# Performance work log

Measured on AMD Instinct MI355X. Metric: run time of the kernel, lower is better.

Reference implementation:

```python
import jax, jax.numpy as jnp
import numpy as np

NUM_HEADS = 16
QKV_FEATURES = 2048
HEAD_DIM = QKV_FEATURES // NUM_HEADS
THETA = 10000.0


def compute_freqs_cis(dim, length, start_pos=0, theta=THETA, dtype=jnp.float32):
    freqs = 1.0 / theta ** (jnp.arange(0, dim, 2, dtype=jnp.float32) / dim)
    t = jnp.arange(length, dtype=jnp.float32) + start_pos
    freqs = jnp.outer(t, freqs)  # (L, dim//2)
    return jnp.sin(freqs).astype(dtype), jnp.cos(freqs).astype(dtype)


def apply_rotary_emb(x, sin, cos):
    # x: (B, L, H, D); sin/cos: (L, D//2); interleaved-pair rotation
    x1 = x[..., 0::2]
    x2 = x[..., 1::2]
    sin = sin[None, :, None, :]
    cos = cos[None, :, None, :]
    y1 = x1 * cos - x2 * sin
    y2 = x1 * sin + x2 * cos
    return jnp.stack([y1, y2], axis=-1).reshape(x.shape)


def setup_inputs() -> dict:
    key = jax.random.key(0)
    ks = jax.random.split(key, 6)
    B, L, E = 2, 2048, 2048
    s_in = 1.0 / np.sqrt(E)
    s_out = 1.0 / np.sqrt(QKV_FEATURES)
    return {
        "x": jax.random.normal(ks[0], (B, L, E), jnp.float32),
        "Wq": jax.random.normal(ks[1], (E, QKV_FEATURES), jnp.float32) * s_in,
        "Wk": jax.random.normal(ks[2], (E, QKV_FEATURES), jnp.float32) * s_in,
        "Wv": jax.random.normal(ks[3], (E, QKV_FEATURES), jnp.float32) * s_in,
        "Wo": jax.random.normal(ks[4], (QKV_FEATURES, E), jnp.float32) * s_out,
        "bo": jnp.zeros((E,), jnp.float32),
    }


def reference(x, Wq, Wk, Wv, Wo, bo):
    B, L, E = x.shape
    H, D = NUM_HEADS, HEAD_DIM

    q = (x @ Wq).reshape(B, L, H, D)
    k = (x @ Wk).reshape(B, L, H, D)
    v = (x @ Wv).reshape(B, L, H, D)

    sin, cos = compute_freqs_cis(D, L)
    q = apply_rotary_emb(q, sin, cos)
    k = apply_rotary_emb(k, sin, cos)

    scale = D ** (-0.5)
    sim = jnp.einsum("bqhd,bkhd->bhqk", q, k) * scale

    pos = jnp.arange(L)
    causal_mask = pos[None, :] <= pos[:, None]  # (Lq, Lk)
    sim = jnp.where(causal_mask[None, None, :, :], sim, -1e9)

    attn = jax.nn.softmax(sim, axis=-1)
    out = jnp.einsum("bhqk,bkhd->bqhd", attn, v).reshape(B, L, H * D)
    return out @ Wo + bo
```

## Files before the change

### kernel.cpp

```cpp
#include <hip/hip_runtime.h>
#include <hip/hip_bf16.h>
#include <stdint.h>
#include <stddef.h>

#define B_   2
#define L_   2048
#define E_   2048
#define H_   16
#define D_   128
#define F_   2048
#define NROW (B_*L_)
#define QS   6144

typedef __bf16 bf16_t;
typedef __bf16 bf16x4 __attribute__((ext_vector_type(4)));
typedef __bf16 bf16x8 __attribute__((ext_vector_type(8)));
typedef float  f32x4  __attribute__((ext_vector_type(4)));

__device__ __forceinline__ void gload16(const void* g, void* l) {
  __builtin_amdgcn_global_load_lds(
      (const __attribute__((address_space(1))) void*)g,
      (__attribute__((address_space(3))) void*)l, 16, 0, 0);
}

__global__ __launch_bounds__(256) void k_convert(const float* __restrict__ in,
                                                 bf16_t* __restrict__ out, int n4) {
  int i = blockIdx.x*256 + threadIdx.x;
  if (i >= n4) return;
  float4 v = ((const float4*)in)[i];
  bf16x4 t;
  t[0] = (__bf16)v.x; t[1] = (__bf16)v.y; t[2] = (__bf16)v.z; t[3] = (__bf16)v.w;
  ((bf16x4*)out)[i] = t;
}

__global__ __launch_bounds__(256) void k_transpose_w(const float* __restrict__ in,
                                                     bf16_t* __restrict__ out) {
  __shared__ float tile[32][33];
  const int ct = blockIdx.x, rt = blockIdx.y;
  const int c = threadIdx.x & 31, r0 = threadIdx.x >> 5;
  #pragma unroll
  for (int k = 0; k < 4; k++) {
    int r = r0 + k*8;
    tile[r][c] = in[(size_t)(rt*32 + r)*2048 + ct*32 + c];
  }
  __syncthreads();
  #pragma unroll
  for (int k = 0; k < 4; k++) {
    int r = r0 + k*8;
    out[(size_t)(ct*32 + r)*2048 + rt*32 + c] = (__bf16)tile[c][r];
  }
}

__global__ __launch_bounds__(256) void k_sincos(float2* __restrict__ sc) {
  int id = blockIdx.x*256 + threadIdx.x;
  int t = id >> 6, i = id & 63;
  float freq = powf(10000.0f, -(float)i / 64.0f);
  float a = (float)t * freq;
  sc[id] = make_float2(cosf(a), sinf(a));
}

__global__ __launch_bounds__(256) void k_rope(bf16_t* __restrict__ qk,
                                              const float2* __restrict__ sc,
                                              float scale, int n4) {
  int i = blockIdx.x*256 + threadIdx.x;
  if (i >= n4) return;
  int e  = i << 2;
  int d  = e & (F_-1);
  int ii = (d & (D_-1)) >> 1;
  int r  = e >> 11;
  int t  = r & (L_-1);
  bf16_t* p = qk + (size_t)r*QS + d;
  bf16x4 v = *(const bf16x4*)p;
  float2 cs0 = sc[t*64 + ii];
  float2 cs1 = sc[t*64 + ii + 1];
  cs0.x *= scale; cs0.y *= scale; cs1.x *= scale; cs1.y *= scale;
  float x0 = (float)v[0], x1 = (float)v[1], x2 = (float)v[2], x3 = (float)v[3];
  bf16x4 o;
  o[0] = (__bf16)(x0*cs0.x - x1*cs0.y);
  o[1] = (__bf16)(x0*cs0.y + x1*cs0.x);
  o[2] = (__bf16)(x2*cs1.x - x3*cs1.y);
  o[3] = (__bf16)(x2*cs1.y + x3*cs1.x);
  *(bf16x4*)p = o;
}

__global__ __launch_bounds__(256) void k_transpose_v(const bf16_t* __restrict__ in,
                                                     bf16_t* __restrict__ out) {
  __shared__ bf16_t tile[32][33];
  const int lt = blockIdx.x, dt = blockIdx.y, bh = blockIdx.z;
  const int b = bh >> 4;
  const int h = bh & 15;
  const int c = threadIdx.x & 31, r0 = threadIdx.x >> 5;
  #pragma unroll
  for (int k = 0; k < 4; k++) {
    int r = r0 + k*8;
    tile[r][c] = in[(size_t)(b*L_ + lt*32 + r)*QS + h*D_ + dt*32 + c];
  }
  __syncthreads();
  #pragma unroll
  for (int k = 0; k < 4; k++) {
    int r = r0 + k*8;
    out[(size_t)(bh*D_ + dt*32 + r)*L_ + lt*32 + c] = tile[c][r];
  }
}

template<typename OutT, bool BIAS>
__global__ __launch_bounds__(256) void k_gemm_bt(const bf16_t* __restrict__ A,
                                                 const bf16_t* __restrict__ BT,
                                                 OutT* __restrict__ C,
                                                 const float* __restrict__ bias,
                                                 int M, int N, int K) {
  __shared__ bf16_t As[128*64];
  __shared__ bf16_t Bs[128*64];
  const int tid  = threadIdx.x;
  const int lane = tid & 63, wave = tid >> 6;
  const int wr = wave >> 1, wc = wave & 1;
  const int nbx = N >> 7, nwg = nbx * (M >> 7);
  int bid = blockIdx.x;
  const int cpx = nwg >> 3;
  bid = (bid & 7)*cpx + (bid >> 3);
  const int bx = bid % nbx, by = bid / nbx;
  const int row0 = by*128, col0 = bx*128;
  const int sr  = tid >> 3;
  const int sxe = ((tid & 7) ^ (sr & 7)) << 3;
  const bf16_t* Ag = A  + (size_t)(row0 + sr)*K + sxe;
  const bf16_t* Bg = BT + (size_t)(col0 + sr)*K + sxe;
  char* AsB = (char*)As; char* BsB = (char*)Bs;
  const int lr = lane & 15, lg = lane >> 4;
  f32x4 acc[4][4] = {};
  for (int kt = 0; kt < K; kt += 64) {
    #pragma unroll
    for (int i = 0; i < 4; i++) {
      gload16(Ag + (size_t)i*32*K + kt, AsB + i*4096 + wave*1024);
      gload16(Bg + (size_t)i*32*K + kt, BsB + i*4096 + wave*1024);
    }
    __syncthreads();
    #pragma unroll
    for (int kd = 0; kd < 2; kd++) {
      bf16x8 af[4], bb[4];
      #pragma unroll
      for (int m = 0; m < 4; m++) {
        const int row = wr*64 + m*16 + lr;
        af[m] = *(const bf16x8*)(AsB + row*128 + (((kd*4 + lg) ^ (lr & 7)) << 4));
      }
      #pragma unroll
      for (int n = 0; n < 4; n++) {
        const int row = wc*64 + n*16 + lr;
        bb[n] = *(const bf16x8*)(BsB + row*128 + (((kd*4 + lg) ^ (lr & 7)) << 4));
      }
      __builtin_amdgcn_s_setprio(1);
      #pragma unroll
      for (int m = 0; m < 4; m++)
        #pragma unroll
        for (int n = 0; n < 4; n++)
          acc[m][n] = __builtin_amdgcn_mfma_f32_16x16x32_bf16(af[m], bb[n], acc[m][n], 0, 0, 0);
      __builtin_amdgcn_s_setprio(0);
    }
    __syncthreads();
  }
  #pragma unroll
  for (int m = 0; m < 4; m++) {
    #pragma unroll
    for (int n = 0; n < 4; n++) {
      const int col = col0 + wc*64 + n*16 + lr;
      const float bv = BIAS ? bias[col] : 0.0f;
      #pragma unroll
      for (int j = 0; j < 4; j++) {
        const int row = row0 + wr*64 + m*16 + lg*4 + j;
        C[(size_t)row*N + col] = (OutT)(acc[m][n][j] + bv);
      }
    }
  }
}

template<bool MASK>
__device__ __forceinline__ void attn_tile(
    int kv0, int wq0, int lr, int lg,
    const char* __restrict__ Kb, const char* __restrict__ Vb, char* __restrict__ Pb,
    const bf16x8 (&aq)[4], f32x4 (&o)[8], float& mrow, float& lsum) {
  const int swz = (lr & 7) << 4;
  f32x4 s[4] = {};
  #pragma unroll
  for (int kd = 0; kd < 4; kd++) {
    bf16x8 ak[4];
    #pragma unroll
    for (int n = 0; n < 4; n++)
      ak[n] = *(const bf16x8*)(Kb + (n*16 + lr)*256 + (((kd*4 + lg) << 4) ^ swz));
    __builtin_amdgcn_s_setprio(1);
    #pragma unroll
    for (int n = 0; n < 4; n++)
      s[n] = __builtin_amdgcn_mfma_f32_16x16x32_bf16(ak[n], aq[kd], s[n], 0, 0, 0);
    __builtin_amdgcn_s_setprio(0);
  }
  if (MASK) {
    const int q = wq0 + lr;
    #pragma unroll
    for (int n = 0; n < 4; n++)
      #pragma unroll
      for (int j = 0; j < 4; j++)
        if (kv0 + n*16 + lg*4 + j > q) s[n][j] = -30000.0f;
  }
  float pmax = fmaxf(
      fmaxf(fmaxf(fmaxf(s[0][0], s[0][1]), fmaxf(s[0][2], s[0][3])),
            fmaxf(fmaxf(s[1][0], s[1][1]), fmaxf(s[1][2], s[1][3]))),
      fmaxf(fmaxf(fmaxf(s[2][0], s[2][1]), fmaxf(s[2][2], s[2][3])),
            fmaxf(fmaxf(s[3][0], s[3][1]), fmaxf(s[3][2], s[3][3]))));
  pmax = fmaxf(pmax, __shfl_xor(pmax, 16));
  pmax = fmaxf(pmax, __shfl_xor(pmax, 32));
  if (!__all(pmax - mrow <= 8.0f)) {
    const float mnew = fmaxf(mrow, pmax);
    const float corr = exp2f(mrow - mnew);
    mrow = mnew;
    lsum *= corr;
    #pragma unroll
    for (int n2 = 0; n2 < 8; n2++) o[n2] *= corr;
  }
  float rs = 0.0f;
  #pragma unroll
  for (int n = 0; n < 4; n++)
    #pragma unroll
    for (int j = 0; j < 4; j++) {
      float p = exp2f(s[n][j] - mrow);
      s[n][j] = p;
      rs += p;
    }
  rs += __shfl_xor(rs, 16);
  rs += __shfl_xor(rs, 32);
  lsum += rs;
  #pragma unroll
  for (int n = 0; n < 4; n++) {
    bf16x4 pw;
    pw[0] = (__bf16)s[n][0]; pw[1] = (__bf16)s[n][1];
    pw[2] = (__bf16)s[n][2]; pw[3] = (__bf16)s[n][3];
    *(bf16x4*)(Pb + ((lr*128 + n*32 + lg*8) ^ swz)) = pw;
  }
  #pragma unroll
  for (int ks = 0; ks < 2; ks++) {
    bf16x8 pb = *(const bf16x8*)(Pb + ((lr*128 + ks*64 + lg*16) ^ swz));
    __builtin_amdgcn_s_setprio(1);
    #pragma unroll
    for (int n2 = 0; n2 < 8; n2++) {
      bf16x8 av = *(const bf16x8*)(Vb + (n2*16 + lr)*128 + (((ks*4 + lg) << 4) ^ swz));
      o[n2] = __builtin_amdgcn_mfma_f32_16x16x32_bf16(av, pb, o[n2], 0, 0, 0);
    }
    __builtin_amdgcn_s_setprio(0);
  }
}

__global__ __launch_bounds__(512, 4) void k_attn(const bf16_t* __restrict__ QKV,
                                                 const bf16_t* __restrict__ Vt,
                                                 bf16_t* __restrict__ O) {
  __shared__ bf16_t Ks[2][64*128];
  __shared__ bf16_t Vs[2][128*64];
  __shared__ bf16_t Pl[8][16*64];
  const int tid = threadIdx.x, lane = tid & 63, wave = tid >> 6;
  const int qt = (int)gridDim.x - 1 - (int)blockIdx.x;
  const int h = blockIdx.y, b = blockIdx.z;
  const int wq0 = qt*128 + wave*16;
  const int lr = lane & 15, lg = lane >> 4;
  char* Pb = (char*)&Pl[wave][0];
  const bf16_t* Q = QKV;
  const bf16_t* K = QKV + F_;

  bf16x8 aq[4];
  #pragma unroll
  for (int kd = 0; kd < 4; kd++)
    aq[kd] = *(const bf16x8*)&Q[(size_t)(b*L_ + wq0 + lr)*QS + h*D_ + kd*32 + lg*8];

  const int kr = tid >> 4, kc = tid & 15;
  const bf16_t* Kg0 = K + (size_t)(b*L_ + kr)*QS + h*D_ + ((kc ^ (kr & 7)) << 3);
  const int vr = tid >> 3, vc = tid & 7;
  const bf16_t* Vg0 = Vt + (size_t)((b*H_ + h)*D_ + vr)*L_ + ((vc ^ (vr & 7)) << 3);

  f32x4 o[8] = {};
  float mrow = -3.0e38f, lsum = 0.0f;
  const int ntb   = 2*qt + 2;
  const int nfull = (wq0 + 1) >> 6;
  const int nmine = ((wq0 + 15) >> 6) + 1;

  {
    char* kb = (char*)&Ks[0][0] + wave*1024;
    char* vb = (char*)&Vs[0][0] + wave*1024;
    gload16(Kg0,                    kb);
    gload16(Kg0 + (size_t)32*QS,    kb + 8192);
    gload16(Vg0,                    vb);
    gload16(Vg0 + (size_t)64*L_,    vb + 8192);
  }
  __syncthreads();

  int buf = 0;
  for (int t = 0; t < ntb; t++) {
    if (t + 1 < ntb) {
      const int kn = (t+1)*64;
      char* kb = (char*)&Ks[buf^1][0] + wave*1024;
      char* vb = (char*)&Vs[buf^1][0] + wave*1024;
      const bf16_t* kg = Kg0 + (size_t)kn*QS;
      const bf16_t* vg = Vg0 + kn;
      gload16(kg,                 kb);
      gload16(kg + (size_t)32*QS, kb + 8192);
      gload16(vg,                 vb);
      gload16(vg + (size_t)64*L_, vb + 8192);
    }
    const char* Kb = (const char*)&Ks[buf][0];
    const char* Vb = (const char*)&Vs[buf][0];
    if (t < nfull)
      attn_tile<false>(t*64, wq0, lr, lg, Kb, Vb, Pb, aq, o, mrow, lsum);
    else if (t < nmine)
      attn_tile<true >(t*64, wq0, lr, lg, Kb, Vb, Pb, aq, o, mrow, lsum);
    __syncthreads();
    buf ^= 1;
  }
  const float inv = 1.0f / lsum;
  bf16_t* orow = O + (size_t)(b*L_ + wq0 + lr)*F_ + h*D_ + lg*4;
  #pragma unroll
  for (int n2 = 0; n2 < 8; n2++) {
    bf16x4 ov;
    ov[0] = (__bf16)(o[n2][0]*inv); ov[1] = (__bf16)(o[n2][1]*inv);
    ov[2] = (__bf16)(o[n2][2]*inv); ov[3] = (__bf16)(o[n2][3]*inv);
    *(bf16x4*)(orow + n2*16) = ov;
  }
}

extern "C" void kernel_launch(void* const* d_in, const int* in_sizes, int n_in,
                              void* d_out, int out_size, void* d_ws, size_t ws_size,
                              hipStream_t stream) {
  const float* x  = (const float*)d_in[0];
  const float* Wq = (const float*)d_in[1];
  const float* Wk = (const float*)d_in[2];
  const float* Wv = (const float*)d_in[3];
  const float* Wo = (const float*)d_in[4];
  const float* bo = (const float*)d_in[5];
  float* out = (float*)d_out;

  char* ws = (char*)d_ws;
  size_t off = 0;
  auto alloc = [&](size_t bytes) {
    char* p = ws + off;
    off = (off + bytes + 255) & ~(size_t)255;
    return p;
  };
  bf16_t* xb    = (bf16_t*)alloc((size_t)NROW*E_*2);
  bf16_t* wqkvt = (bf16_t*)alloc((size_t)3*F_*E_*2);
  bf16_t* wot   = (bf16_t*)alloc((size_t)F_*E_*2);
  float2* sc    = (float2*)alloc((size_t)L_*64*sizeof(float2));
  bf16_t* qkv   = (bf16_t*)alloc((size_t)NROW*QS*2);
  bf16_t* vt    = (bf16_t*)alloc((size_t)NROW*F_*2);
  bf16_t* ob    = xb;

  const float scale2 = 0.08838834764831845f * 1.44269504088896f;

  k_convert<<<dim3((NROW*E_/4 + 255)/256), 256, 0, stream>>>(x, xb, NROW*E_/4);
  k_transpose_w<<<dim3(64, 64), 256, 0, stream>>>(Wq, wqkvt);
  k_transpose_w<<<dim3(64, 64), 256, 0, stream>>>(Wk, wqkvt + (size_t)F_*E_);
  k_transpose_w<<<dim3(64, 64), 256, 0, stream>>>(Wv, wqkvt + (size_t)2*F_*E_);
  k_transpose_w<<<dim3(64, 64), 256, 0, stream>>>(Wo, wot);
  k_sincos<<<dim3(L_*64/256), 256, 0, stream>>>(sc);

  k_gemm_bt<bf16_t, false><<<dim3((QS/128)*(NROW/128)), 256, 0, stream>>>(
      xb, wqkvt, qkv, nullptr, NROW, QS, E_);

  k_rope<<<dim3((NROW*F_/4 + 255)/256), 256, 0, stream>>>(qkv,      sc, scale2, NROW*F_/4);
  k_rope<<<dim3((NROW*F_/4 + 255)/256), 256, 0, stream>>>(qkv + F_, sc, 1.0f,   NROW*F_/4);
  k_transpose_v<<<dim3(L_/32, D_/32, B_*H_), 256, 0, stream>>>(qkv + 2*F_, vt);

  k_attn<<<dim3(L_/128, H_, B_), 512, 0, stream>>>(qkv, vt, ob);

  k_gemm_bt<float, true><<<dim3((E_/128)*(NROW/128)), 256, 0, stream>>>(
      ob, wot, out, bo, NROW, E_, F_);
}
```

Measured before the change: 438.8 us.

## Triple-buffer GEMM K-loop with async LDS loads and merge small launches

The bf16 GEMM is restructured to use a 32-wide K step with a three-stage LDS ring buffer, issuing global-to-LDS loads two steps ahead and waiting with explicit vmcnt counts instead of a full sync per tile. Occupancy is hinted at three blocks per CU, and the LDS swizzle is adjusted to the narrower rows. Separately, the four weight-transpose launches are merged into one 3D grid and the two RoPE launches into one kernel, cutting launch overhead. The hand-written waitcnt and barrier scheme relies on the exact number of outstanding loads, so a miscount would break correctness.

New measurement: 443.3 us. No clear change (+1.0%).

```diff
diff --git a/kernel.cpp b/kernel.cpp
--- a/kernel.cpp
+++ b/kernel.cpp
@@ -23,6 +23,8 @@
       (__attribute__((address_space(3))) void*)l, 16, 0, 0);
 }
 
+#define VMC(n)  asm volatile("s_waitcnt vmcnt(" #n ")" ::: "memory")
+
 __global__ __launch_bounds__(256) void k_convert(const float* __restrict__ in,
                                                  bf16_t* __restrict__ out, int n4) {
   int i = blockIdx.x*256 + threadIdx.x;
@@ -33,9 +35,16 @@
   ((bf16x4*)out)[i] = t;
 }
 
-__global__ __launch_bounds__(256) void k_transpose_w(const float* __restrict__ in,
-                                                     bf16_t* __restrict__ out) {
+__global__ __launch_bounds__(256) void k_transpose_w4(const float* __restrict__ Wq,
+                                                      const float* __restrict__ Wk,
+                                                      const float* __restrict__ Wv,
+                                                      const float* __restrict__ Wo,
+                                                      bf16_t* __restrict__ wqkvt,
+                                                      bf16_t* __restrict__ wot) {
   __shared__ float tile[32][33];
+  const int z = blockIdx.z;
+  const float* in = (z == 0) ? Wq : (z == 1) ? Wk : (z == 2) ? Wv : Wo;
+  bf16_t* out = (z < 3) ? wqkvt + (size_t)z*F_*E_ : wot;
   const int ct = blockIdx.x, rt = blockIdx.y;
   const int c = threadIdx.x & 31, r0 = threadIdx.x >> 5;
   #pragma unroll
@@ -59,17 +68,19 @@
   sc[id] = make_float2(cosf(a), sinf(a));
 }
 
-__global__ __launch_bounds__(256) void k_rope(bf16_t* __restrict__ qk,
-                                              const float2* __restrict__ sc,
-                                              float scale, int n4) {
+__global__ __launch_bounds__(256) void k_rope2(bf16_t* __restrict__ qkv,
+                                               const float2* __restrict__ sc,
+                                               float qscale, int half) {
   int i = blockIdx.x*256 + threadIdx.x;
-  if (i >= n4) return;
-  int e  = i << 2;
+  const int part = (i >= half);
+  int j = part ? i - half : i;
+  int e  = j << 2;
   int d  = e & (F_-1);
   int ii = (d & (D_-1)) >> 1;
   int r  = e >> 11;
   int t  = r & (L_-1);
-  bf16_t* p = qk + (size_t)r*QS + d;
+  bf16_t* p = qkv + (size_t)r*QS + part*F_ + d;
+  const float scale = part ? 1.0f : qscale;
   bf16x4 v = *(const bf16x4*)p;
   float2 cs0 = sc[t*64 + ii];
   float2 cs1 = sc[t*64 + ii + 1];
@@ -104,58 +115,62 @@
 }
 
 template<typename OutT, bool BIAS>
-__global__ __launch_bounds__(256) void k_gemm_bt(const bf16_t* __restrict__ A,
-                                                 const bf16_t* __restrict__ BT,
-                                                 OutT* __restrict__ C,
-                                                 const float* __restrict__ bias,
-                                                 int M, int N, int K) {
-  __shared__ bf16_t As[128*64];
-  __shared__ bf16_t Bs[128*64];
-  const int tid  = threadIdx.x;
-  const int lane = tid & 63, wave = tid >> 6;
+__global__ __launch_bounds__(256, 3) void k_gemm_bt(const bf16_t* __restrict__ A,
+                                                    const bf16_t* __restrict__ BT,
+                                                    OutT* __restrict__ C,
+                                                    const float* __restrict__ bias,
+                                                    int M, int N, int K) {
+  __shared__ char sm[49152];
+  const int tid = threadIdx.x, lane = tid & 63, wave = tid >> 6;
   const int wr = wave >> 1, wc = wave & 1;
+  const int lr = lane & 15, lg = lane >> 4;
   const int nbx = N >> 7, nwg = nbx * (M >> 7);
   int bid = blockIdx.x;
   const int cpx = nwg >> 3;
   bid = (bid & 7)*cpx + (bid >> 3);
   const int bx = bid % nbx, by = bid / nbx;
-  const int row0 = by*128, col0 = bx*128;
-  const int sr  = tid >> 3;
-  const int sxe = ((tid & 7) ^ (sr & 7)) << 3;
+  const int row0 = by << 7, col0 = bx << 7;
+  const int sr  = tid >> 2;
+  const int sxe = (((tid & 3) ^ ((sr >> 1) & 3)) << 3);
   const bf16_t* Ag = A  + (size_t)(row0 + sr)*K + sxe;
   const bf16_t* Bg = BT + (size_t)(col0 + sr)*K + sxe;
-  char* AsB = (char*)As; char* BsB = (char*)Bs;
-  const int lr = lane & 15, lg = lane >> 4;
+  const int dst0 = wave*1024;
+  auto stage = [&](int t) {
+    char* base = sm + (t % 3)*16384;
+    const bf16_t* a = Ag + t*32;
+    const bf16_t* b = Bg + t*32;
+    gload16(a,                base + dst0);
+    gload16(a + (size_t)64*K, base + 4096  + dst0);
+    gload16(b,                base + 8192  + dst0);
+    gload16(b + (size_t)64*K, base + 12288 + dst0);
+  };
+  const int cs   = (lg ^ ((lr >> 1) & 3)) << 4;
+  const int arow = (wr*64 + lr)*64;
+  const int brow = 8192 + (wc*64 + lr)*64;
   f32x4 acc[4][4] = {};
-  for (int kt = 0; kt < K; kt += 64) {
-    #pragma unroll
-    for (int i = 0; i < 4; i++) {
-      gload16(Ag + (size_t)i*32*K + kt, AsB + i*4096 + wave*1024);
-      gload16(Bg + (size_t)i*32*K + kt, BsB + i*4096 + wave*1024);
-    }
-    __syncthreads();
-    #pragma unroll
-    for (int kd = 0; kd < 2; kd++) {
-      bf16x8 af[4], bb[4];
+  stage(0); stage(1);
+  const int nt = K >> 5;
+  for (int t = 0; t < nt; t++) {
+    if (t + 2 < nt)      { stage(t + 2); VMC(8); }
+    else if (t + 1 < nt) { VMC(4); }
+    else                 { VMC(0); }
+    __builtin_amdgcn_s_barrier();
+    const char* base = sm + (t % 3)*16384;
+    bf16x8 af[4], bb[4];
+    #pragma unroll
+    for (int m = 0; m < 4; m++) af[m] = *(const bf16x8*)(base + arow + m*1024 + cs);
+    #pragma unroll
+    for (int n = 0; n < 4; n++) bb[n] = *(const bf16x8*)(base + brow + n*1024 + cs);
+    asm volatile("s_waitcnt lgkmcnt(0)" ::: "memory");
+    __builtin_amdgcn_sched_barrier(0);
+    __builtin_amdgcn_s_setprio(1);
+    #pragma unroll
+    for (int m = 0; m < 4; m++)
       #pragma unroll
-      for (int m = 0; m < 4; m++) {
-        const int row = wr*64 + m*16 + lr;
-        af[m] = *(const bf16x8*)(AsB + row*128 + (((kd*4 + lg) ^ (lr & 7)) << 4));
-      }
-      #pragma unroll
-      for (int n = 0; n < 4; n++) {
-        const int row = wc*64 + n*16 + lr;
-        bb[n] = *(const bf16x8*)(BsB + row*128 + (((kd*4 + lg) ^ (lr & 7)) << 4));
-      }
-      __builtin_amdgcn_s_setprio(1);
-      #pragma unroll
-      for (int m = 0; m < 4; m++)
-        #pragma unroll
-        for (int n = 0; n < 4; n++)
-          acc[m][n] = __builtin_amdgcn_mfma_f32_16x16x32_bf16(af[m], bb[n], acc[m][n], 0, 0, 0);
-      __builtin_amdgcn_s_setprio(0);
-    }
-    __syncthreads();
+      for (int n = 0; n < 4; n++)
+        acc[m][n] = __builtin_amdgcn_mfma_f32_16x16x32_bf16(af[m], bb[n], acc[m][n], 0, 0, 0);
+    __builtin_amdgcn_s_setprio(0);
+    __builtin_amdgcn_s_barrier();
   }
   #pragma unroll
   for (int m = 0; m < 4; m++) {
@@ -280,10 +295,10 @@
   {
     char* kb = (char*)&Ks[0][0] + wave*1024;
     char* vb = (char*)&Vs[0][0] + wave*1024;
-    gload16(Kg0,                    kb);
-    gload16(Kg0 + (size_t)32*QS,    kb + 8192);
-    gload16(Vg0,                    vb);
-    gload16(Vg0 + (size_t)64*L_,    vb + 8192);
+    gload16(Kg0,                 kb);
+    gload16(Kg0 + (size_t)32*QS, kb + 8192);
+    gload16(Vg0,                 vb);
+    gload16(Vg0 + (size_t)64*L_, vb + 8192);
   }
   __syncthreads();
 
@@ -349,17 +364,13 @@
   const float scale2 = 0.08838834764831845f * 1.44269504088896f;
 
   k_convert<<<dim3((NROW*E_/4 + 255)/256), 256, 0, stream>>>(x, xb, NROW*E_/4);
-  k_transpose_w<<<dim3(64, 64), 256, 0, stream>>>(Wq, wqkvt);
-  k_transpose_w<<<dim3(64, 64), 256, 0, stream>>>(Wk, wqkvt + (size_t)F_*E_);
-  k_transpose_w<<<dim3(64, 64), 256, 0, stream>>>(Wv, wqkvt + (size_t)2*F_*E_);
-  k_transpose_w<<<dim3(64, 64), 256, 0, stream>>>(Wo, wot);
+  k_transpose_w4<<<dim3(64, 64, 4), 256, 0, stream>>>(Wq, Wk, Wv, Wo, wqkvt, wot);
   k_sincos<<<dim3(L_*64/256), 256, 0, stream>>>(sc);
 
   k_gemm_bt<bf16_t, false><<<dim3((QS/128)*(NROW/128)), 256, 0, stream>>>(
       xb, wqkvt, qkv, nullptr, NROW, QS, E_);
 
-  k_rope<<<dim3((NROW*F_/4 + 255)/256), 256, 0, stream>>>(qkv,      sc, scale2, NROW*F_/4);
-  k_rope<<<dim3((NROW*F_/4 + 255)/256), 256, 0, stream>>>(qkv + F_, sc, 1.0f,   NROW*F_/4);
+  k_rope2<<<dim3(2*(NROW*F_/4)/256), 256, 0, stream>>>(qkv, sc, scale2, NROW*F_/4);
   k_transpose_v<<<dim3(L_/32, D_/32, B_*H_), 256, 0, stream>>>(qkv + 2*F_, vt);
 
   k_attn<<<dim3(L_/128, H_, B_), 512, 0, stream>>>(qkv, vt, ob);
```
